# Kernel optimization log

Hardware: AMD Instinct MI355X
Metric: run time of the kernel (lower is better)

Reference implementation:

```python
import jax, jax.numpy as jnp
import numpy as np

N = 100000   # total nodes (users + items)
D = 256      # in_channels == out_channels
E = 1000000  # directed edges
C = 64       # number of clusters


def setup_inputs() -> dict:
    key = jax.random.key(0)
    k1, k2, k3, k4, k5 = jax.random.split(key, 5)
    X = jax.random.normal(k1, (N, D), jnp.float32)
    weight = jax.random.normal(k2, (D, D), jnp.float32) / np.sqrt(D).astype(np.float32)
    bias = jax.random.normal(k3, (D,), jnp.float32) * 0.01
    cluster_assignment = jax.random.randint(k4, (N,), 0, C)
    edge_index = jax.random.randint(k5, (2, E), 0, N)
    return {"X": X, "weight": weight, "bias": bias,
            "cluster_assignment": cluster_assignment, "edge_index": edge_index}


def reference(X, weight, bias, cluster_assignment, edge_index):
    # Per-cluster GCNConv == whole-graph GCNConv restricted to intra-cluster
    # edges (edges crossing clusters are masked out), with self-loops added
    # per node. Clusters with zero intra-cluster edges are skipped and keep
    # the original X (the Python loop `continue`s).
    src, dst = edge_index[0], edge_index[1]
    intra = (cluster_assignment[src] == cluster_assignment[dst]).astype(X.dtype)

    # GCN symmetric normalization with self-loops: deg = A_intra deg + 1
    deg = jax.ops.segment_sum(intra, dst, num_segments=N) + 1.0
    dinv = jax.lax.rsqrt(deg)                      # deg >= 1 always
    norm = dinv[src] * dinv[dst] * intra           # zero on cross-cluster edges

    Xl = X @ weight                                # [N, D] linear transform
    agg = jax.ops.segment_sum(norm[:, None] * Xl[src], dst, num_segments=N)
    agg = agg + (dinv * dinv)[:, None] * Xl        # self-loop contribution
    out = agg + bias

    # Clusters with no internal edges are left untouched by the torch loop.
    edges_per_cluster = jax.ops.segment_sum(intra, cluster_assignment[dst], num_segments=C)
    active = edges_per_cluster[cluster_assignment] > 0  # [N] bool
    return jnp.where(active[:, None], out, X)
```

## Files before the change

### kernel.cpp

```cpp
#include <hip/hip_runtime.h>

#define D 256

typedef float f32x4 __attribute__((ext_vector_type(4)));
typedef _Float16 f16x8 __attribute__((ext_vector_type(8)));

__global__ void k_edges(const int* __restrict__ ei, const int* __restrict__ cl,
                        float* __restrict__ degx, int E) {
    int e = blockIdx.x * blockDim.x + threadIdx.x;
    if (e >= E) return;
    int s = ei[e];
    int d = ei[E + e];
    if (cl[s] == cl[d])
        unsafeAtomicAdd(&degx[d], 1.0f);
}

__global__ void k_active(const float* __restrict__ degx, const int* __restrict__ cl,
                         int* __restrict__ activeC, int N) {
    int i = blockIdx.x * blockDim.x + threadIdx.x;
    if (i < N && degx[i] > 0.0f) activeC[cl[i]] = 1;
}

__global__ void k_init(const float* __restrict__ X, const float* __restrict__ degx,
                       float* __restrict__ out, int N) {
    int i = blockIdx.x * blockDim.x + threadIdx.x;
    int lane = threadIdx.x & 63;
    float dx = 0.0f;
    bool hit = false;
    if (i < N) { dx = degx[i]; hit = dx > 0.0f; }
    unsigned long long m = __ballot(hit);
    int base = i - lane;
    while (m) {
        int b = __ffsll((long long)m) - 1;
        m &= m - 1;
        int r = base + b;
        float inv = 1.0f / (__shfl(dx, b) + 1.0f);
        float4 x = *(const float4*)(X + (size_t)r * D + lane * 4);
        x.x *= inv; x.y *= inv; x.z *= inv; x.w *= inv;
        *(float4*)(out + (size_t)r * D + lane * 4) = x;
    }
}

__global__ void k_scatter(const int* __restrict__ ei, const int* __restrict__ cl,
                          const float* __restrict__ degx, const float* __restrict__ X,
                          float* __restrict__ out, int E) {
    int e = blockIdx.x * blockDim.x + threadIdx.x;
    int lane = threadIdx.x & 63;
    int s = 0, d = 0;
    bool intra = false;
    if (e < E) {
        s = ei[e];
        d = ei[E + e];
        intra = (cl[s] == cl[d]);
    }
    unsigned long long mask = __ballot(intra);
    while (mask) {
        int b = __ffsll((long long)mask) - 1;
        mask &= mask - 1;
        int ss = __shfl(s, b);
        int dd = __shfl(d, b);
        float norm = rsqrtf((degx[ss] + 1.0f) * (degx[dd] + 1.0f));
        float4 xv = *(const float4*)(X + (size_t)ss * D + lane * 4);
        float* op = out + (size_t)dd * D + lane * 4;
        unsafeAtomicAdd(op + 0, norm * xv.x);
        unsafeAtomicAdd(op + 1, norm * xv.y);
        unsafeAtomicAdd(op + 2, norm * xv.z);
        unsafeAtomicAdd(op + 3, norm * xv.w);
    }
}

__global__ void k_prepw(const float* __restrict__ W, _Float16* __restrict__ Wp) {
    int idx = blockIdx.x * blockDim.x + threadIdx.x;
    if (idx >= D * D) return;
    int k = idx >> 8, n = idx & 255;
    int ks = k >> 5, kk = k & 31;
    int h = kk >> 3, i = kk & 7;
    int ct = n >> 4, cn = n & 15;
    int lane = h * 16 + cn;
    Wp[(((ks * 16 + ct) * 64 + lane) << 3) + i] = (_Float16)W[idx];
}

__global__ __launch_bounds__(1024, 4) void k_gemm(
        const _Float16* __restrict__ Wp, const float* __restrict__ bias,
        const float* __restrict__ X, const float* __restrict__ degx,
        const int* __restrict__ cl, const int* __restrict__ activeC,
        float* __restrict__ out, int N) {
    extern __shared__ _Float16 Wl[];
    int tid  = threadIdx.x;
    int lane = tid & 63;
    int wid  = tid >> 6;
    int rA = lane & 15;
    int h  = lane >> 4;
    int cn = lane & 15;

    {
        const char* src = (const char*)Wp + tid * 16;
        #pragma unroll
        for (int it = 0; it < 8; ++it) {
            __builtin_amdgcn_global_load_lds(
                (const __attribute__((address_space(1))) void*)(src + it * 16384),
                (__attribute__((address_space(3))) void*)((char*)Wl + tid * 16 + it * 16384),
                16, 0, 0);
        }
    }
    float bv[16];
    #pragma unroll
    for (int ct = 0; ct < 16; ++ct) bv[ct] = bias[ct * 16 + cn];
    __syncthreads();

    int T = (N + 15) >> 4;
    for (int t = (int)blockIdx.x * 16 + wid; t < T; t += 4096) {
        long r = (long)t * 16 + rA;
        if (r > (long)N - 1) r = (long)N - 1;
        const float* arow = ((degx[r] > 0.0f) ? out : X) + r * D;

        f32x4 acc[16];
        #pragma unroll
        for (int ct = 0; ct < 16; ++ct) acc[ct] = (f32x4){0.f, 0.f, 0.f, 0.f};

        #pragma unroll
        for (int ks = 0; ks < 8; ++ks) {
            const float* ap = arow + ks * 32 + h * 8;
            float4 a0 = *(const float4*)(ap);
            float4 a1 = *(const float4*)(ap + 4);
            f16x8 af;
            af[0] = (_Float16)a0.x; af[1] = (_Float16)a0.y;
            af[2] = (_Float16)a0.z; af[3] = (_Float16)a0.w;
            af[4] = (_Float16)a1.x; af[5] = (_Float16)a1.y;
            af[6] = (_Float16)a1.z; af[7] = (_Float16)a1.w;
            #pragma unroll
            for (int ct = 0; ct < 16; ++ct) {
                f16x8 wf = *(const f16x8*)&Wl[(((ks * 16 + ct) * 64) + lane) << 3];
                acc[ct] = __builtin_amdgcn_mfma_f32_16x16x32_f16(af, wf, acc[ct], 0, 0, 0);
            }
        }

        #pragma unroll
        for (int j = 0; j < 4; ++j) {
            long rr = (long)t * 16 + h * 4 + j;
            bool ok = rr < (long)N;
            long rc = ok ? rr : (long)N - 1;
            bool act = activeC[cl[rc]] != 0;
            unsigned long long bad = __ballot(!act || !ok);
            float* orow = out + rc * D;
            if (bad == 0ULL) {
                #pragma unroll
                for (int ct = 0; ct < 16; ++ct)
                    orow[ct * 16 + cn] = acc[ct][j] + bv[ct];
            } else if (ok) {
                const float* xrow = X + rc * D;
                #pragma unroll
                for (int ct = 0; ct < 16; ++ct) {
                    float v = acc[ct][j] + bv[ct];
                    if (!act) v = xrow[ct * 16 + cn];
                    orow[ct * 16 + cn] = v;
                }
            }
        }
    }
}

extern "C" void kernel_launch(void* const* d_in, const int* in_sizes, int n_in,
                              void* d_out, int out_size, void* d_ws, size_t ws_size,
                              hipStream_t stream) {
    const float* X    = (const float*)d_in[0];
    const float* W    = (const float*)d_in[1];
    const float* bias = (const float*)d_in[2];
    const int*   cl   = (const int*)d_in[3];
    const int*   ei   = (const int*)d_in[4];
    int N = in_sizes[3];
    int E = in_sizes[4] / 2;
    float* out = (float*)d_out;

    char* ws = (char*)d_ws;
    float* degx = (float*)ws;
    size_t off = ((size_t)N * sizeof(float) + 255) & ~(size_t)255;
    int* activeC = (int*)(ws + off);
    size_t zbytes = off + 256;
    _Float16* Wp = (_Float16*)(ws + ((zbytes + 255) & ~(size_t)255));

    hipFuncSetAttribute((const void*)k_gemm,
                        hipFuncAttributeMaxDynamicSharedMemorySize, 131072);

    hipMemsetAsync(ws, 0, zbytes, stream);
    k_prepw<<<(D * D + 255) / 256, 256, 0, stream>>>(W, Wp);
    k_edges<<<(E + 255) / 256, 256, 0, stream>>>(ei, cl, degx, E);
    k_active<<<(N + 255) / 256, 256, 0, stream>>>(degx, cl, activeC, N);
    k_init<<<(N + 255) / 256, 256, 0, stream>>>(X, degx, out, N);
    k_scatter<<<(E + 255) / 256, 256, 0, stream>>>(ei, cl, degx, X, out, E);
    k_gemm<<<256, 1024, 131072, stream>>>(Wp, bias, X, degx, cl, activeC, out, N);
}
```

Measured before the change: 143.8 us.

## Software-pipeline GEMM A loads, split columns per wave, fuse active-cluster marking

The GEMM now splits each 16-row tile into two 128-column halves handled by different waves. Each wave prefetches the next tile's A row into registers during the MFMA loop, and the next row's degx one iteration earlier. MFMA operands are swapped so each lane holds four consecutive output columns of one row. That gives float4 stores, and bias is preloaded from LDS into the accumulators. The separate k_active launch is folded into k_init to save one launch. The costs are higher register pressure, A rows being read twice (once per column half), and a leftover dead code block.

```diff
diff --git a/kernel.cpp b/kernel.cpp
--- a/kernel.cpp
+++ b/kernel.cpp
@@ -15,19 +15,18 @@
         unsafeAtomicAdd(&degx[d], 1.0f);
 }
 
-__global__ void k_active(const float* __restrict__ degx, const int* __restrict__ cl,
-                         int* __restrict__ activeC, int N) {
-    int i = blockIdx.x * blockDim.x + threadIdx.x;
-    if (i < N && degx[i] > 0.0f) activeC[cl[i]] = 1;
-}
-
 __global__ void k_init(const float* __restrict__ X, const float* __restrict__ degx,
+                       const int* __restrict__ cl, int* __restrict__ activeC,
                        float* __restrict__ out, int N) {
     int i = blockIdx.x * blockDim.x + threadIdx.x;
     int lane = threadIdx.x & 63;
     float dx = 0.0f;
     bool hit = false;
-    if (i < N) { dx = degx[i]; hit = dx > 0.0f; }
+    if (i < N) {
+        dx = degx[i];
+        hit = dx > 0.0f;
+        if (hit) activeC[cl[i]] = 1;
+    }
     unsigned long long m = __ballot(hit);
     int base = i - lane;
     while (m) {
@@ -85,78 +84,135 @@
         const float* __restrict__ X, const float* __restrict__ degx,
         const int* __restrict__ cl, const int* __restrict__ activeC,
         float* __restrict__ out, int N) {
-    extern __shared__ _Float16 Wl[];
-    int tid  = threadIdx.x;
+    extern __shared__ char smem[];
+    _Float16* Wl = (_Float16*)smem;
+    float* Bl = (float*)(smem + 131072);
+
+    int tid = threadIdx.x;
     int lane = tid & 63;
     int wid  = tid >> 6;
     int rA = lane & 15;
     int h  = lane >> 4;
-    int cn = lane & 15;
-
+
+    if (tid < 256) Bl[tid] = bias[tid];
     {
         const char* src = (const char*)Wp + tid * 16;
         #pragma unroll
         for (int it = 0; it < 8; ++it) {
             __builtin_amdgcn_global_load_lds(
                 (const __attribute__((address_space(1))) void*)(src + it * 16384),
-                (__attribute__((address_space(3))) void*)((char*)Wl + tid * 16 + it * 16384),
+                (__attribute__((address_space(3))) void*)(smem + tid * 16 + it * 16384),
                 16, 0, 0);
         }
     }
-    float bv[16];
-    #pragma unroll
-    for (int ct = 0; ct < 16; ++ct) bv[ct] = bias[ct * 16 + cn];
     __syncthreads();
 
-    int T = (N + 15) >> 4;
-    for (int t = (int)blockIdx.x * 16 + wid; t < T; t += 4096) {
-        long r = (long)t * 16 + rA;
-        if (r > (long)N - 1) r = (long)N - 1;
-        const float* arow = ((degx[r] > 0.0f) ? out : X) + r * D;
-
-        f32x4 acc[16];
-        #pragma unroll
-        for (int ct = 0; ct < 16; ++ct) acc[ct] = (f32x4){0.f, 0.f, 0.f, 0.f};
+    const int T2 = ((N + 15) >> 4) << 1;
+    const int STRIDE = 4096;
+
+    int t = (int)blockIdx.x * 16 + wid;
+    if (t >= T2) return;
+    const int half = t & 1;
+    const int colbase = half * 128 + h * 4;
+
+    {
+        long r0 = (long)(t >> 1) * 16 + rA;
+        if (r0 > (long)N - 1) r0 = (long)N - 1;
+        const float* arow0 = ((degx[r0] > 0.0f) ? out : X) + r0 * D;
+        (void)arow0;
+    }
+
+    f16x8 curA[8];
+    float4 Pa[4], Pb[4];
+    {
+        long r0 = (long)(t >> 1) * 16 + rA;
+        if (r0 > (long)N - 1) r0 = (long)N - 1;
+        const float* arow0 = ((degx[r0] > 0.0f) ? out : X) + r0 * D;
+        #pragma unroll
+        for (int ks = 0; ks < 4; ++ks) {
+            float4 a0 = *(const float4*)(arow0 + ks * 32 + h * 8);
+            float4 a1 = *(const float4*)(arow0 + ks * 32 + h * 8 + 4);
+            f16x8 af;
+            af[0]=(_Float16)a0.x; af[1]=(_Float16)a0.y; af[2]=(_Float16)a0.z; af[3]=(_Float16)a0.w;
+            af[4]=(_Float16)a1.x; af[5]=(_Float16)a1.y; af[6]=(_Float16)a1.z; af[7]=(_Float16)a1.w;
+            curA[ks] = af;
+        }
+        #pragma unroll
+        for (int s = 0; s < 4; ++s) {
+            Pa[s] = *(const float4*)(arow0 + (4 + s) * 32 + h * 8);
+            Pb[s] = *(const float4*)(arow0 + (4 + s) * 32 + h * 8 + 4);
+        }
+    }
+
+    int tn = t + STRIDE;
+    int tnc = (tn < T2) ? tn : 0;
+    long rn = (long)(tnc >> 1) * 16 + rA;
+    float dgxN = degx[rn];
+
+    const char* WlB = (const char*)Wl + lane * 16;
+
+    for (;;) {
+        const int tile = t >> 1;
+        const float* arowN = ((dgxN > 0.0f) ? out : X) + rn * D;
+
+        int t2 = t + 2 * STRIDE;
+        int t2c = (t2 < T2) ? t2 : 0;
+        long r2 = (long)(t2c >> 1) * 16 + rA;
+        float dgx2 = degx[r2];
+
+        long rr = (long)tile * 16 + rA;
+        long rc = (rr < (long)N) ? rr : (long)N - 1;
+        int act = activeC[cl[rc]];
+        unsigned long long bad = __ballot(act == 0 || rr >= (long)N);
+
+        f32x4 acc[8];
+        #pragma unroll
+        for (int c = 0; c < 8; ++c)
+            acc[c] = *(const f32x4*)(Bl + colbase + c * 16);
 
         #pragma unroll
         for (int ks = 0; ks < 8; ++ks) {
-            const float* ap = arow + ks * 32 + h * 8;
-            float4 a0 = *(const float4*)(ap);
-            float4 a1 = *(const float4*)(ap + 4);
-            f16x8 af;
-            af[0] = (_Float16)a0.x; af[1] = (_Float16)a0.y;
-            af[2] = (_Float16)a0.z; af[3] = (_Float16)a0.w;
-            af[4] = (_Float16)a1.x; af[5] = (_Float16)a1.y;
-            af[6] = (_Float16)a1.z; af[7] = (_Float16)a1.w;
+            const int s = ks & 3;
+            {
+                float4 a0 = Pa[s], a1 = Pb[s];
+                f16x8 af;
+                af[0]=(_Float16)a0.x; af[1]=(_Float16)a0.y; af[2]=(_Float16)a0.z; af[3]=(_Float16)a0.w;
+                af[4]=(_Float16)a1.x; af[5]=(_Float16)a1.y; af[6]=(_Float16)a1.z; af[7]=(_Float16)a1.w;
+                curA[(ks >= 4) ? (ks - 4) : (ks + 4)] = af;
+            }
+            Pa[s] = *(const float4*)(arowN + ks * 32 + h * 8);
+            Pb[s] = *(const float4*)(arowN + ks * 32 + h * 8 + 4);
+            f16x8 af = curA[ks];
             #pragma unroll
-            for (int ct = 0; ct < 16; ++ct) {
-                f16x8 wf = *(const f16x8*)&Wl[(((ks * 16 + ct) * 64) + lane) << 3];
-                acc[ct] = __builtin_amdgcn_mfma_f32_16x16x32_f16(af, wf, acc[ct], 0, 0, 0);
+            for (int c = 0; c < 8; ++c) {
+                f16x8 wf = *(const f16x8*)(WlB + (size_t)(ks * 16 + half * 8 + c) * 1024);
+                acc[c] = __builtin_amdgcn_mfma_f32_16x16x32_f16(wf, af, acc[c], 0, 0, 0);
             }
         }
 
-        #pragma unroll
-        for (int j = 0; j < 4; ++j) {
-            long rr = (long)t * 16 + h * 4 + j;
-            bool ok = rr < (long)N;
-            long rc = ok ? rr : (long)N - 1;
-            bool act = activeC[cl[rc]] != 0;
-            unsigned long long bad = __ballot(!act || !ok);
-            float* orow = out + rc * D;
-            if (bad == 0ULL) {
-                #pragma unroll
-                for (int ct = 0; ct < 16; ++ct)
-                    orow[ct * 16 + cn] = acc[ct][j] + bv[ct];
-            } else if (ok) {
-                const float* xrow = X + rc * D;
-                #pragma unroll
-                for (int ct = 0; ct < 16; ++ct) {
-                    float v = acc[ct][j] + bv[ct];
-                    if (!act) v = xrow[ct * 16 + cn];
-                    orow[ct * 16 + cn] = v;
-                }
+        float* orow = out + rc * D + colbase;
+        if (bad == 0ULL) {
+            #pragma unroll
+            for (int c = 0; c < 8; ++c)
+                *(float4*)(orow + c * 16) =
+                    (float4){acc[c][0], acc[c][1], acc[c][2], acc[c][3]};
+        } else if (rr < (long)N) {
+            const float* xrow = X + rc * D + colbase;
+            #pragma unroll
+            for (int c = 0; c < 8; ++c) {
+                float4 v;
+                if (act) v = (float4){acc[c][0], acc[c][1], acc[c][2], acc[c][3]};
+                else     v = *(const float4*)(xrow + c * 16);
+                *(float4*)(orow + c * 16) = v;
             }
         }
+
+        t = tn;
+        if (t >= T2) break;
+        tn = t + STRIDE;
+        tnc = (tn < T2) ? tn : 0;
+        rn = (long)(tnc >> 1) * 16 + rA;
+        dgxN = dgx2;
     }
 }
 
@@ -180,13 +236,12 @@
     _Float16* Wp = (_Float16*)(ws + ((zbytes + 255) & ~(size_t)255));
 
     hipFuncSetAttribute((const void*)k_gemm,
-                        hipFuncAttributeMaxDynamicSharedMemorySize, 131072);
+                        hipFuncAttributeMaxDynamicSharedMemorySize, 135168);
 
     hipMemsetAsync(ws, 0, zbytes, stream);
     k_prepw<<<(D * D + 255) / 256, 256, 0, stream>>>(W, Wp);
     k_edges<<<(E + 255) / 256, 256, 0, stream>>>(ei, cl, degx, E);
-    k_active<<<(N + 255) / 256, 256, 0, stream>>>(degx, cl, activeC, N);
-    k_init<<<(N + 255) / 256, 256, 0, stream>>>(X, degx, out, N);
+    k_init<<<(N + 255) / 256, 256, 0, stream>>>(X, degx, cl, activeC, out, N);
     k_scatter<<<(E + 255) / 256, 256, 0, stream>>>(ei, cl, degx, X, out, E);
-    k_gemm<<<256, 1024, 131072, stream>>>(Wp, bias, X, degx, cl, activeC, out, N);
-}
+    k_gemm<<<256, 1024, 132096, stream>>>(Wp, bias, X, degx, cl, activeC, out, N);
+}
```

Result: slower. 417.8 us, median of 2 (+190.6%).

## Fuse active-cluster marking into init and transpose MFMA output for vector stores

Applied to the files above, without the earlier changes.

Removes the separate k_active launch by marking active clusters inside k_init. In the GEMM, the MFMA operands are swapped so each lane holds four consecutive output columns of one row. That allows float4 stores and a single per-row activity check instead of four scalar-store passes. Bias is staged in LDS and preloaded into the accumulators, and the next A-row chunk is loaded one step ahead. The cost is a little more LDS and more live registers for the prefetch.

```diff
diff --git a/kernel.cpp b/kernel.cpp
--- a/kernel.cpp
+++ b/kernel.cpp
@@ -15,19 +15,18 @@
         unsafeAtomicAdd(&degx[d], 1.0f);
 }
 
-__global__ void k_active(const float* __restrict__ degx, const int* __restrict__ cl,
-                         int* __restrict__ activeC, int N) {
-    int i = blockIdx.x * blockDim.x + threadIdx.x;
-    if (i < N && degx[i] > 0.0f) activeC[cl[i]] = 1;
-}
-
 __global__ void k_init(const float* __restrict__ X, const float* __restrict__ degx,
+                       const int* __restrict__ cl, int* __restrict__ activeC,
                        float* __restrict__ out, int N) {
     int i = blockIdx.x * blockDim.x + threadIdx.x;
     int lane = threadIdx.x & 63;
     float dx = 0.0f;
     bool hit = false;
-    if (i < N) { dx = degx[i]; hit = dx > 0.0f; }
+    if (i < N) {
+        dx = degx[i];
+        hit = dx > 0.0f;
+        if (hit) activeC[cl[i]] = 1;
+    }
     unsigned long long m = __ballot(hit);
     int base = i - lane;
     while (m) {
@@ -85,76 +84,75 @@
         const float* __restrict__ X, const float* __restrict__ degx,
         const int* __restrict__ cl, const int* __restrict__ activeC,
         float* __restrict__ out, int N) {
-    extern __shared__ _Float16 Wl[];
-    int tid  = threadIdx.x;
+    extern __shared__ char smem[];
+    _Float16* Wl = (_Float16*)smem;
+    float* Bl = (float*)(smem + 131072);
+
+    int tid = threadIdx.x;
     int lane = tid & 63;
     int wid  = tid >> 6;
     int rA = lane & 15;
     int h  = lane >> 4;
-    int cn = lane & 15;
 
+    if (tid < 256) Bl[tid] = bias[tid];
     {
         const char* src = (const char*)Wp + tid * 16;
         #pragma unroll
         for (int it = 0; it < 8; ++it) {
             __builtin_amdgcn_global_load_lds(
                 (const __attribute__((address_space(1))) void*)(src + it * 16384),
-                (__attribute__((address_space(3))) void*)((char*)Wl + tid * 16 + it * 16384),
+                (__attribute__((address_space(3))) void*)(smem + tid * 16 + it * 16384),
                 16, 0, 0);
         }
     }
-    float bv[16];
-    #pragma unroll
-    for (int ct = 0; ct < 16; ++ct) bv[ct] = bias[ct * 16 + cn];
     __syncthreads();
 
     int T = (N + 15) >> 4;
     for (int t = (int)blockIdx.x * 16 + wid; t < T; t += 4096) {
-        long r = (long)t * 16 + rA;
-        if (r > (long)N - 1) r = (long)N - 1;
-        const float* arow = ((degx[r] > 0.0f) ? out : X) + r * D;
+        long rr = (long)t * 16 + rA;
+        long rc = (rr < (long)N) ? rr : (long)N - 1;
+        const float* arow = ((degx[rc] > 0.0f) ? out : X) + rc * D;
+        int act = activeC[cl[rc]];
+        unsigned long long bad = __ballot(act == 0 || rr >= (long)N);
 
         f32x4 acc[16];
         #pragma unroll
-        for (int ct = 0; ct < 16; ++ct) acc[ct] = (f32x4){0.f, 0.f, 0.f, 0.f};
+        for (int ct = 0; ct < 16; ++ct)
+            acc[ct] = *(const f32x4*)(Bl + ct * 16 + h * 4);
 
+        float4 Pa = *(const float4*)(arow + h * 8);
+        float4 Pb = *(const float4*)(arow + h * 8 + 4);
         #pragma unroll
         for (int ks = 0; ks < 8; ++ks) {
-            const float* ap = arow + ks * 32 + h * 8;
-            float4 a0 = *(const float4*)(ap);
-            float4 a1 = *(const float4*)(ap + 4);
+            float4 a0 = Pa, a1 = Pb;
+            if (ks < 7) {
+                Pa = *(const float4*)(arow + (ks + 1) * 32 + h * 8);
+                Pb = *(const float4*)(arow + (ks + 1) * 32 + h * 8 + 4);
+            }
             f16x8 af;
-            af[0] = (_Float16)a0.x; af[1] = (_Float16)a0.y;
-            af[2] = (_Float16)a0.z; af[3] = (_Float16)a0.w;
-            af[4] = (_Float16)a1.x; af[5] = (_Float16)a1.y;
-            af[6] = (_Float16)a1.z; af[7] = (_Float16)a1.w;
+            af[0]=(_Float16)a0.x; af[1]=(_Float16)a0.y; af[2]=(_Float16)a0.z; af[3]=(_Float16)a0.w;
+            af[4]=(_Float16)a1.x; af[5]=(_Float16)a1.y; af[6]=(_Float16)a1.z; af[7]=(_Float16)a1.w;
             #pragma unroll
             for (int ct = 0; ct < 16; ++ct) {
                 f16x8 wf = *(const f16x8*)&Wl[(((ks * 16 + ct) * 64) + lane) << 3];
-                acc[ct] = __builtin_amdgcn_mfma_f32_16x16x32_f16(af, wf, acc[ct], 0, 0, 0);
+                acc[ct] = __builtin_amdgcn_mfma_f32_16x16x32_f16(wf, af, acc[ct], 0, 0, 0);
             }
         }
 
-        #pragma unroll
-        for (int j = 0; j < 4; ++j) {
-            long rr = (long)t * 16 + h * 4 + j;
-            bool ok = rr < (long)N;
-            long rc = ok ? rr : (long)N - 1;
-            bool act = activeC[cl[rc]] != 0;
-            unsigned long long bad = __ballot(!act || !ok);
-            float* orow = out + rc * D;
-            if (bad == 0ULL) {
-                #pragma unroll
-                for (int ct = 0; ct < 16; ++ct)
-                    orow[ct * 16 + cn] = acc[ct][j] + bv[ct];
-            } else if (ok) {
-                const float* xrow = X + rc * D;
-                #pragma unroll
-                for (int ct = 0; ct < 16; ++ct) {
-                    float v = acc[ct][j] + bv[ct];
-                    if (!act) v = xrow[ct * 16 + cn];
-                    orow[ct * 16 + cn] = v;
-                }
+        float* orow = out + rc * D + h * 4;
+        if (bad == 0ULL) {
+            #pragma unroll
+            for (int ct = 0; ct < 16; ++ct)
+                *(float4*)(orow + ct * 16) =
+                    (float4){acc[ct][0], acc[ct][1], acc[ct][2], acc[ct][3]};
+        } else if (rr < (long)N) {
+            const float* xrow = X + rc * D + h * 4;
+            #pragma unroll
+            for (int ct = 0; ct < 16; ++ct) {
+                float4 v;
+                if (act) v = (float4){acc[ct][0], acc[ct][1], acc[ct][2], acc[ct][3]};
+                else     v = *(const float4*)(xrow + ct * 16);
+                *(float4*)(orow + ct * 16) = v;
             }
         }
     }
@@ -180,13 +178,12 @@
     _Float16* Wp = (_Float16*)(ws + ((zbytes + 255) & ~(size_t)255));
 
     hipFuncSetAttribute((const void*)k_gemm,
-                        hipFuncAttributeMaxDynamicSharedMemorySize, 131072);
+                        hipFuncAttributeMaxDynamicSharedMemorySize, 135168);
 
     hipMemsetAsync(ws, 0, zbytes, stream);
     k_prepw<<<(D * D + 255) / 256, 256, 0, stream>>>(W, Wp);
     k_edges<<<(E + 255) / 256, 256, 0, stream>>>(ei, cl, degx, E);
-    k_active<<<(N + 255) / 256, 256, 0, stream>>>(degx, cl, activeC, N);
-    k_init<<<(N + 255) / 256, 256, 0, stream>>>(X, degx, out, N);
+    k_init<<<(N + 255) / 256, 256, 0, stream>>>(X, degx, cl, activeC, out, N);
     k_scatter<<<(E + 255) / 256, 256, 0, stream>>>(ei, cl, degx, X, out, E);
-    k_gemm<<<256, 1024, 131072, stream>>>(Wp, bias, X, degx, cl, activeC, out, N);
+    k_gemm<<<256, 1024, 132096, stream>>>(Wp, bias, X, degx, cl, activeC, out, N);
 }
```

New measurement: 495.4 us. 3.45x slower.
